# Kernel optimization log

Measured on AMD Instinct MI355X. Metric: run time of the kernel, lower is better.

## Reference

```python
import jax, jax.numpy as jnp
import numpy as np


def setup_inputs() -> dict:
    key = jax.random.key(0)
    ks = jax.random.split(key, 8)
    N, E, H, C, L, G = 100000, 1600000, 128, 10, 5, 64
    x = jax.random.normal(ks[0], (N, H), dtype=jnp.float32)
    edge_index = jax.random.randint(ks[1], (2, E), 0, N, dtype=jnp.int32)
    batch = jnp.sort(jax.random.randint(ks[2], (N,), 0, G, dtype=jnp.int32))
    # Glorot-ish init scale for stability
    Ws = jax.random.normal(ks[3], (L, H, H), dtype=jnp.float32) * (1.0 / np.sqrt(H))
    bs = jax.random.normal(ks[4], (L, H), dtype=jnp.float32) * 0.01
    W_out = jax.random.normal(ks[5], (H, C), dtype=jnp.float32) * (1.0 / np.sqrt(H))
    b_out = jax.random.normal(ks[6], (C,), dtype=jnp.float32) * 0.01
    return {"x": x, "edge_index": edge_index, "batch": batch, "num_graphs": G,
            "Ws": Ws, "bs": bs, "W_out": W_out, "b_out": b_out}


def reference(x, edge_index, batch, num_graphs, Ws, bs, W_out, b_out):
    N = x.shape[0]
    # --- GCN normalization (add self-loops, symmetric deg^-1/2 norm), computed once ---
    loop = jnp.arange(N, dtype=edge_index.dtype)
    src = jnp.concatenate([edge_index[0], loop])  # message sources (x_j)
    dst = jnp.concatenate([edge_index[1], loop])  # aggregation targets
    deg = jax.ops.segment_sum(jnp.ones_like(dst, dtype=x.dtype), dst, num_segments=N)
    dis = jnp.where(deg > 0, jax.lax.rsqrt(jnp.maximum(deg, 1.0)), 0.0)
    norm = dis[src] * dis[dst]  # [E+N]
    # --- stacked GCNConv + ReLU ---
    for l in range(Ws.shape[0]):
        xw = x @ Ws[l]                                   # [N, H] dense transform
        msg = norm[:, None] * xw[src]                    # gather + scale per edge
        x = jax.nn.relu(jax.ops.segment_sum(msg, dst, num_segments=N) + bs[l])
    # --- global mean pool over graphs ---
    sums = jax.ops.segment_sum(x, batch, num_segments=num_graphs)       # [G, H]
    cnts = jax.ops.segment_sum(jnp.ones((N,), x.dtype), batch, num_segments=num_graphs)
    pooled = sums / jnp.maximum(cnts, 1.0)[:, None]
    return pooled @ W_out + b_out
```

## Files before the change

kernel.cpp:

```cpp
#include <hip/hip_runtime.h>
#include <hip/hip_bf16.h>
#include <stdint.h>

#define HDIM 128
#define SBITS 10
#define SBMAX 128

typedef __attribute__((ext_vector_type(8))) short short8;
typedef __attribute__((ext_vector_type(4))) float f32x4;

__device__ __forceinline__ ushort f2bf(float f) {
  uint u = __float_as_uint(f);
  u = (u + 0x7fffu + ((u >> 16) & 1u)) >> 16;
  return (ushort)u;
}
__device__ __forceinline__ float bflo(uint v) { return __uint_as_float(v << 16); }
__device__ __forceinline__ float bfhi(uint v) { return __uint_as_float(v & 0xffff0000u); }

__device__ __forceinline__ int pdeg4(int c) { return (c + 4) & ~3; }

__device__ __forceinline__ uint pack_cw(int src, float w) {
  uint w15 = (__float_as_uint(w) + 0x8000u) >> 16;
  return (uint)src | (w15 << 17);
}
__device__ __forceinline__ uint cw_src(uint u) { return u & 0x1FFFFu; }
__device__ __forceinline__ float cw_w(uint u) { return __uint_as_float((u >> 17) << 16); }


__global__ __launch_bounds__(256) void bucket_edges(const int* __restrict__ ei,
                                                    int* __restrict__ bktcur,
                                                    uint* __restrict__ bkt, int E,
                                                    int cap) {
  __shared__ int hist[SBMAX], base[SBMAX];
  const int t = threadIdx.x;
  const int c0 = blockIdx.x * 2048;
  for (int i = t; i < SBMAX; i += 256) hist[i] = 0;
  __syncthreads();
  uint pk[8];
  int sb_[8], rk[8];
#pragma unroll
  for (int j = 0; j < 8; ++j) {
    int idx = c0 + j * 256 + t;
    sb_[j] = -1;
    if (idx < E) {
      int s = ei[idx];
      int d = ei[E + idx];
      int b = d >> SBITS;
      pk[j] = (uint)(d & 1023) | ((uint)s << SBITS);
      sb_[j] = b;
      rk[j] = atomicAdd(&hist[b], 1);
    }
  }
  __syncthreads();
  for (int i = t; i < SBMAX; i += 256)
    base[i] = hist[i] ? atomicAdd(&bktcur[i * 16], hist[i]) : 0;
  __syncthreads();
#pragma unroll
  for (int j = 0; j < 8; ++j)
    if (sb_[j] >= 0)
      bkt[(size_t)sb_[j] * cap + base[sb_[j]] + rk[j]] = pk[j];
}

__global__ __launch_bounds__(256) void csr_count(const uint* __restrict__ bkt,
                                                 const int* __restrict__ bktcur,
                                                 float* __restrict__ dis,
                                                 int* __restrict__ sbtot, int cap,
                                                 int N) {
  __shared__ int cnt[1024];
  __shared__ int red[256];
  const int sb = blockIdx.x, t = threadIdx.x;
  const int n0 = sb << SBITS;
  const int ecnt = bktcur[sb * 16];
  const uint* eb = bkt + (size_t)sb * cap;
  for (int i = t; i < 1024; i += 256) cnt[i] = 0;
  __syncthreads();
  for (int i = t; i < ecnt; i += 256)
    atomicAdd(&cnt[__builtin_nontemporal_load(eb + i) & 1023], 1);
  __syncthreads();
  int s = 0;
#pragma unroll
  for (int j = 0; j < 4; ++j) {
    int idx = t * 4 + j, n = n0 + idx;
    if (n < N) {
      dis[n] = rsqrtf((float)(cnt[idx] + 1));
      s += pdeg4(cnt[idx]);
    }
  }
  red[t] = s;
  __syncthreads();
  for (int off = 128; off; off >>= 1) {
    if (t < off) red[t] += red[t + off];
    __syncthreads();
  }
  if (t == 0) sbtot[sb] = red[0];
}

__global__ __launch_bounds__(128) void scan_sb(const int* __restrict__ sbtot,
                                               int* __restrict__ sbbase,
                                               int* __restrict__ rowptr, int SB,
                                               int N) {
  __shared__ int sh[128];
  int t = threadIdx.x;
  int v = (t < SB) ? sbtot[t] : 0;
  sh[t] = v;
  __syncthreads();
  for (int off = 1; off < 128; off <<= 1) {
    int add = (t >= off) ? sh[t - off] : 0;
    __syncthreads();
    sh[t] += add;
    __syncthreads();
  }
  if (t < SB) sbbase[t] = sh[t] - v;
  if (t == 127) rowptr[N] = sh[127];
}

__global__ __launch_bounds__(256) void csr_place(const uint* __restrict__ bkt,
                                                 const int* __restrict__ bktcur,
                                                 const int* __restrict__ sbbase,
                                                 const float* __restrict__ dis,
                                                 int* __restrict__ rowptr,
                                                 uint* __restrict__ colw, int cap,
                                                 int N) {
  __shared__ int cnt[1024], cur[1024];
  __shared__ int sh[256];
  const int sb = blockIdx.x, t = threadIdx.x;
  const int n0 = sb << SBITS;
  const int ecnt = bktcur[sb * 16];
  const uint* eb = bkt + (size_t)sb * cap;
  const int base = sbbase[sb];
  for (int i = t; i < 1024; i += 256) cnt[i] = 0;
  __syncthreads();
  for (int i = t; i < ecnt; i += 256)
    atomicAdd(&cnt[__builtin_nontemporal_load(eb + i) & 1023], 1);
  __syncthreads();
  int v[4], tsum = 0;
#pragma unroll
  for (int j = 0; j < 4; ++j) {
    int idx = t * 4 + j, n = n0 + idx;
    v[j] = (n < N) ? pdeg4(cnt[idx]) : 0;
    tsum += v[j];
  }
  sh[t] = tsum;
  __syncthreads();
  for (int off = 1; off < 256; off <<= 1) {
    int add = (t >= off) ? sh[t - off] : 0;
    __syncthreads();
    sh[t] += add;
    __syncthreads();
  }
  int p = sh[t] - tsum;
#pragma unroll
  for (int j = 0; j < 4; ++j) {
    int idx = t * 4 + j, n = n0 + idx;
    if (n < N) {
      rowptr[n] = base + p;
      cur[idx] = p + 1;
      float dn = dis[n];
      colw[base + p] = pack_cw(n, dn * dn);
      int deg = cnt[idx];
      for (int q = deg + 1; q < v[j]; ++q) colw[base + p + q] = (uint)n;
    }
    p += v[j];
  }
  __syncthreads();
  for (int i = t; i < ecnt; i += 256) {
    uint u = __builtin_nontemporal_load(eb + i);
    int dloc = (int)(u & 1023);
    int s2 = (int)(u >> SBITS);
    int pos = atomicAdd(&cur[dloc], 1);
    int d = n0 + dloc;
    colw[base + pos] = pack_cw(s2, dis[s2] * dis[d]);
  }
}

__global__ __launch_bounds__(256) void swz_w(const float* __restrict__ Ws,
                                             ushort* __restrict__ Wsw, int total) {
  int idx = blockIdx.x * 256 + threadIdx.x;
  if (idx >= total) return;
  int l = idx >> 14, r = idx & 16383;
  int j = r & 7, lane = (r >> 3) & 63, kk = (r >> 9) & 3, c = r >> 11;
  int n = c * 16 + (lane & 15);
  int k = kk * 32 + (lane >> 4) * 8 + j;
  Wsw[idx] = f2bf(Ws[l * 16384 + k * HDIM + n]);
}


template <bool F32IN>
__global__ __launch_bounds__(256) void gemm_kernel(const void* __restrict__ Xin,
                                                   const ushort* __restrict__ Wsw,
                                                   ushort* __restrict__ XW, int N,
                                                   int ntiles) {
  __shared__ ushort wlds[16384];
  __shared__ ushort clds[64 * 136];
  const int t = threadIdx.x;
  {
    const int4* src = (const int4*)Wsw;
    int4* dst = (int4*)wlds;
#pragma unroll
    for (int i = 0; i < 8; ++i) dst[t + 256 * i] = src[t + 256 * i];
  }
  __syncthreads();

  const int wave = t >> 6, lane = t & 63;
  const int kq = lane >> 4;

  for (int tile = blockIdx.x; tile < ntiles; tile += gridDim.x) {
    const int row0 = tile * 64 + wave * 16 + (lane & 15);
    const bool inb = row0 < N;

    short8 afr[4];
#pragma unroll
    for (int kk = 0; kk < 4; ++kk) afr[kk] = short8{0, 0, 0, 0, 0, 0, 0, 0};
    if (inb) {
      if constexpr (F32IN) {
        const float* arow = (const float*)Xin + (size_t)row0 * HDIM;
#pragma unroll
        for (int kk = 0; kk < 4; ++kk) {
          float4 x0 = *(const float4*)(arow + kk * 32 + kq * 8);
          float4 x1 = *(const float4*)(arow + kk * 32 + kq * 8 + 4);
          short8 f;
          f[0] = (short)f2bf(x0.x); f[1] = (short)f2bf(x0.y);
          f[2] = (short)f2bf(x0.z); f[3] = (short)f2bf(x0.w);
          f[4] = (short)f2bf(x1.x); f[5] = (short)f2bf(x1.y);
          f[6] = (short)f2bf(x1.z); f[7] = (short)f2bf(x1.w);
          afr[kk] = f;
        }
      } else {
        const short8* arow = (const short8*)((const ushort*)Xin + (size_t)row0 * HDIM);
#pragma unroll
        for (int kk = 0; kk < 4; ++kk) afr[kk] = arow[kk * 4 + kq];
      }
    }

    f32x4 acc[8];
#pragma unroll
    for (int c = 0; c < 8; ++c) acc[c] = f32x4{0.f, 0.f, 0.f, 0.f};
#pragma unroll
    for (int kk = 0; kk < 4; ++kk) {
#pragma unroll
      for (int c = 0; c < 8; ++c) {
        short8 bfr = *(const short8*)(wlds + (((c * 4 + kk) * 64 + lane) << 3));
        acc[c] = __builtin_amdgcn_mfma_f32_16x16x32_bf16(afr[kk], bfr, acc[c], 0, 0, 0);
      }
    }

    __syncthreads();
    const int m0 = wave * 16 + kq * 4;
#pragma unroll
    for (int c = 0; c < 8; ++c) {
      int col = c * 16 + (lane & 15);
#pragma unroll
      for (int r = 0; r < 4; ++r) clds[(m0 + r) * 136 + col] = f2bf(acc[c][r]);
    }
    __syncthreads();
#pragma unroll
    for (int i = 0; i < 4; ++i) {
      int idx = t + 256 * i;
      int row = idx >> 4, piece = idx & 15;
      int grow = tile * 64 + row;
      if (grow < N)
        ((int4*)XW)[(size_t)tile * 1024 + idx] =
            *(const int4*)(clds + row * 136 + piece * 8);
    }
  }
}

__global__ __launch_bounds__(256, 6) void agg_kernel(const ushort* __restrict__ XW,
                                                     const uint* __restrict__ colw,
                                                     const int* __restrict__ rowptr,
                                                     const float* __restrict__ bias,
                                                     ushort* __restrict__ Y, int N) {
  const int lane = threadIdx.x & 63;
  const int node = blockIdx.x * 4 + (threadIdx.x >> 6);
  if (node >= N) return;
  const int e = lane >> 4, c = lane & 15;
  const int beg = rowptr[node];
  const int pdeg = rowptr[node + 1] - beg;
  const int last = pdeg - 1;

  uint cw[6];
#pragma unroll
  for (int k = 0; k < 6; ++k) {
    int off = 4 * k + e;
    cw[k] = __builtin_nontemporal_load(colw + beg + (off < pdeg ? off : last));
  }
  uint4 gv[6];
#pragma unroll
  for (int k = 0; k < 6; ++k)
    gv[k] = *(const uint4*)(XW + ((size_t)cw_src(cw[k]) << 7) + c * 8);

  float acc[8];
#pragma unroll
  for (int i = 0; i < 8; ++i) acc[i] = 0.f;

#pragma unroll
  for (int k = 0; k < 6; ++k) {
    int off = 4 * k + e;
    float w = (off < pdeg) ? cw_w(cw[k]) : 0.f;
    uint4 v = gv[k];
    acc[0] += w * bflo(v.x); acc[1] += w * bfhi(v.x);
    acc[2] += w * bflo(v.y); acc[3] += w * bfhi(v.y);
    acc[4] += w * bflo(v.z); acc[5] += w * bfhi(v.z);
    acc[6] += w * bflo(v.w); acc[7] += w * bfhi(v.w);
  }
  for (int off = 24 + e; off < pdeg; off += 4) {
    uint u = __builtin_nontemporal_load(colw + beg + off);
    uint4 v = *(const uint4*)(XW + ((size_t)cw_src(u) << 7) + c * 8);
    float w = cw_w(u);
    acc[0] += w * bflo(v.x); acc[1] += w * bfhi(v.x);
    acc[2] += w * bflo(v.y); acc[3] += w * bfhi(v.y);
    acc[4] += w * bflo(v.z); acc[5] += w * bfhi(v.z);
    acc[6] += w * bflo(v.w); acc[7] += w * bfhi(v.w);
  }

#pragma unroll
  for (int i = 0; i < 8; ++i) {
    acc[i] += __shfl_xor(acc[i], 16, 64);
    acc[i] += __shfl_xor(acc[i], 32, 64);
  }
  if (e == 0) {
    float4 b0 = *(const float4*)(bias + c * 8);
    float4 b1 = *(const float4*)(bias + c * 8 + 4);
    uint4 pk;
    pk.x = (uint)f2bf(fmaxf(acc[0] + b0.x, 0.f)) | ((uint)f2bf(fmaxf(acc[1] + b0.y, 0.f)) << 16);
    pk.y = (uint)f2bf(fmaxf(acc[2] + b0.z, 0.f)) | ((uint)f2bf(fmaxf(acc[3] + b0.w, 0.f)) << 16);
    pk.z = (uint)f2bf(fmaxf(acc[4] + b1.x, 0.f)) | ((uint)f2bf(fmaxf(acc[5] + b1.y, 0.f)) << 16);
    pk.w = (uint)f2bf(fmaxf(acc[6] + b1.z, 0.f)) | ((uint)f2bf(fmaxf(acc[7] + b1.w, 0.f)) << 16);
    *(uint4*)(Y + (size_t)node * HDIM + c * 8) = pk;
  }
}


__global__ __launch_bounds__(256) void pool_partial(const ushort* __restrict__ x,
                                                    const int* __restrict__ batch,
                                                    float* __restrict__ pooled,
                                                    int* __restrict__ gcnt, int N) {
  const int g = blockIdx.x, s = blockIdx.y;
  const int t = threadIdx.x;
  __shared__ int range[2];
  __shared__ float sums[256];
  if (t < 2) {
    int target = g + t;
    int lo = 0, hi = N;
    while (lo < hi) {
      int mid = (lo + hi) >> 1;
      if (batch[mid] < target) lo = mid + 1;
      else hi = mid;
    }
    range[t] = lo;
  }
  __syncthreads();
  int beg = range[0], end = range[1];
  if (s == 0 && t == 0) gcnt[g] = end - beg;
  int col = t & 127, half = t >> 7;
  float acc = 0.f;
  for (int n = beg + s * 2 + half; n < end; n += 16) {
    acc += __uint_as_float(((uint)x[(size_t)n * HDIM + col]) << 16);
  }
  sums[t] = acc;
  __syncthreads();
  if (t < 128) atomicAdd(&pooled[g * HDIM + t], sums[t] + sums[t + 128]);
}

__global__ __launch_bounds__(256) void out_final(const float* __restrict__ pooled,
                                                 const int* __restrict__ gcnt,
                                                 const float* __restrict__ W_out,
                                                 const float* __restrict__ b_out,
                                                 float* __restrict__ out, int G, int C) {
  int i = blockIdx.x * 256 + threadIdx.x;
  if (i >= G * C) return;
  int g = i / C, c = i - g * C;
  float inv = 1.f / (float)max(gcnt[g], 1);
  const float* pg = pooled + g * HDIM;
  float o = 0.f;
  for (int h = 0; h < HDIM; ++h) o += pg[h] * W_out[h * C + c];
  out[i] = b_out[c] + o * inv;
}


extern "C" void kernel_launch(void* const* d_in, const int* in_sizes, int n_in,
                              void* d_out, int out_size, void* d_ws, size_t ws_size,
                              hipStream_t stream) {
  (void)n_in;
  (void)ws_size;
  const float* x = (const float*)d_in[0];
  const int* ei = (const int*)d_in[1];
  const int* batch = (const int*)d_in[2];
  const float* Ws = (const float*)d_in[4];
  const float* bs = (const float*)d_in[5];
  const float* W_out = (const float*)d_in[6];
  const float* b_out = (const float*)d_in[7];
  float* out = (float*)d_out;

  const int N = in_sizes[0] / HDIM;
  const int E = in_sizes[1] / 2;
  const int L = in_sizes[5] / HDIM;
  const int C = in_sizes[7];
  const int G = out_size / C;
  const int SB = (N + 1023) >> SBITS;
  const int cap = E / SB + 8192;

  char* p = (char*)d_ws;
  auto carve = [&](size_t bytes) {
    char* r = p;
    p += (bytes + 255) & ~(size_t)255;
    return r;
  };
  int* bktcur = (int*)carve(SBMAX * 64);
  float* dis = (float*)carve((size_t)N * 4);
  int* rowptr = (int*)carve((size_t)(N + 1) * 4);
  int* sbtot = (int*)carve(SBMAX * 4);
  int* sbbase = (int*)carve(SBMAX * 4);
  uint* bkt = (uint*)carve((size_t)SB * cap * 4);
  uint* colw = (uint*)carve(((size_t)E + 4 * (size_t)N + 64) * 4);
  ushort* Wsw = (ushort*)carve((size_t)L * HDIM * HDIM * 2);
  ushort* xw = (ushort*)carve((size_t)N * HDIM * 2);
  ushort* y0 = (ushort*)carve((size_t)N * HDIM * 2);
  ushort* y1 = (ushort*)carve((size_t)N * HDIM * 2);
  float* pooled = (float*)carve((size_t)G * HDIM * 4 + (size_t)G * 4);
  int* gcnt = (int*)(pooled + (size_t)G * HDIM);

  hipMemsetAsync(bktcur, 0, SBMAX * 64, stream);
  hipMemsetAsync(pooled, 0, (size_t)G * HDIM * 4 + (size_t)G * 4, stream);

  bucket_edges<<<(E + 2047) / 2048, 256, 0, stream>>>(ei, bktcur, bkt, E, cap);
  csr_count<<<SB, 256, 0, stream>>>(bkt, bktcur, dis, sbtot, cap, N);
  scan_sb<<<1, 128, 0, stream>>>(sbtot, sbbase, rowptr, SB, N);
  csr_place<<<SB, 256, 0, stream>>>(bkt, bktcur, sbbase, dis, rowptr, colw, cap, N);
  swz_w<<<(L * HDIM * HDIM + 255) / 256, 256, 0, stream>>>(Ws, Wsw, L * HDIM * HDIM);

  const int ntiles = (N + 63) / 64;
  const int gb = 768;
  gemm_kernel<true><<<gb, 256, 0, stream>>>(x, Wsw, xw, N, ntiles);
  agg_kernel<<<(N + 3) / 4, 256, 0, stream>>>(xw, colw, rowptr, bs, y0, N);
  ushort* xc = y0;
  ushort* xn = y1;
  for (int l = 1; l < L; ++l) {
    gemm_kernel<false><<<gb, 256, 0, stream>>>(xc, Wsw + (size_t)l * HDIM * HDIM, xw, N, ntiles);
    agg_kernel<<<(N + 3) / 4, 256, 0, stream>>>(xw, colw, rowptr, bs + (size_t)l * HDIM, xn, N);
    ushort* tmp = xc;
    xc = xn;
    xn = tmp;
  }
  pool_partial<<<dim3(G, 8), 256, 0, stream>>>(xc, batch, pooled, gcnt, N);
  out_final<<<(G * C + 255) / 256, 256, 0, stream>>>(pooled, gcnt, W_out, b_out, out, G, C);
}
```

Baseline: 573.5 us.

## Fuse aggregation and GEMM per layer by reassociating A(XW) as (AX)W

Uses linearity to aggregate the input features first and then apply the weight matrix in the same kernel. Each block gathers 64 nodes into LDS, with a two-node software pipeline that overlaps gathers, then runs the MFMA GEMM and applies bias plus ReLU before writing out. This removes the intermediate XW round trip through global memory and one launch per layer, and the input is converted to bf16 once up front. In exchange, occupancy drops (launch bounds 3, large LDS footprint), each block must reload the weights, and the GEMM now runs on a bf16-rounded aggregate, which changes rounding.

```diff
diff --git a/kernel.cpp b/kernel.cpp
--- a/kernel.cpp
+++ b/kernel.cpp
@@ -184,149 +184,155 @@
   Wsw[idx] = f2bf(Ws[l * 16384 + k * HDIM + n]);
 }
 
-
-template <bool F32IN>
-__global__ __launch_bounds__(256) void gemm_kernel(const void* __restrict__ Xin,
-                                                   const ushort* __restrict__ Wsw,
-                                                   ushort* __restrict__ XW, int N,
-                                                   int ntiles) {
-  __shared__ ushort wlds[16384];
-  __shared__ ushort clds[64 * 136];
-  const int t = threadIdx.x;
-  {
-    const int4* src = (const int4*)Wsw;
-    int4* dst = (int4*)wlds;
-#pragma unroll
-    for (int i = 0; i < 8; ++i) dst[t + 256 * i] = src[t + 256 * i];
-  }
-  __syncthreads();
-
-  const int wave = t >> 6, lane = t & 63;
-  const int kq = lane >> 4;
-
-  for (int tile = blockIdx.x; tile < ntiles; tile += gridDim.x) {
-    const int row0 = tile * 64 + wave * 16 + (lane & 15);
-    const bool inb = row0 < N;
-
-    short8 afr[4];
-#pragma unroll
-    for (int kk = 0; kk < 4; ++kk) afr[kk] = short8{0, 0, 0, 0, 0, 0, 0, 0};
-    if (inb) {
-      if constexpr (F32IN) {
-        const float* arow = (const float*)Xin + (size_t)row0 * HDIM;
-#pragma unroll
-        for (int kk = 0; kk < 4; ++kk) {
-          float4 x0 = *(const float4*)(arow + kk * 32 + kq * 8);
-          float4 x1 = *(const float4*)(arow + kk * 32 + kq * 8 + 4);
-          short8 f;
-          f[0] = (short)f2bf(x0.x); f[1] = (short)f2bf(x0.y);
-          f[2] = (short)f2bf(x0.z); f[3] = (short)f2bf(x0.w);
-          f[4] = (short)f2bf(x1.x); f[5] = (short)f2bf(x1.y);
-          f[6] = (short)f2bf(x1.z); f[7] = (short)f2bf(x1.w);
-          afr[kk] = f;
-        }
-      } else {
-        const short8* arow = (const short8*)((const ushort*)Xin + (size_t)row0 * HDIM);
-#pragma unroll
-        for (int kk = 0; kk < 4; ++kk) afr[kk] = arow[kk * 4 + kq];
-      }
-    }
-
-    f32x4 acc[8];
-#pragma unroll
-    for (int c = 0; c < 8; ++c) acc[c] = f32x4{0.f, 0.f, 0.f, 0.f};
-#pragma unroll
-    for (int kk = 0; kk < 4; ++kk) {
-#pragma unroll
-      for (int c = 0; c < 8; ++c) {
-        short8 bfr = *(const short8*)(wlds + (((c * 4 + kk) * 64 + lane) << 3));
-        acc[c] = __builtin_amdgcn_mfma_f32_16x16x32_bf16(afr[kk], bfr, acc[c], 0, 0, 0);
-      }
-    }
-
-    __syncthreads();
-    const int m0 = wave * 16 + kq * 4;
-#pragma unroll
-    for (int c = 0; c < 8; ++c) {
-      int col = c * 16 + (lane & 15);
-#pragma unroll
-      for (int r = 0; r < 4; ++r) clds[(m0 + r) * 136 + col] = f2bf(acc[c][r]);
-    }
-    __syncthreads();
-#pragma unroll
-    for (int i = 0; i < 4; ++i) {
-      int idx = t + 256 * i;
-      int row = idx >> 4, piece = idx & 15;
-      int grow = tile * 64 + row;
-      if (grow < N)
-        ((int4*)XW)[(size_t)tile * 1024 + idx] =
-            *(const int4*)(clds + row * 136 + piece * 8);
-    }
-  }
-}
-
-__global__ __launch_bounds__(256, 6) void agg_kernel(const ushort* __restrict__ XW,
-                                                     const uint* __restrict__ colw,
-                                                     const int* __restrict__ rowptr,
-                                                     const float* __restrict__ bias,
-                                                     ushort* __restrict__ Y, int N) {
-  const int lane = threadIdx.x & 63;
-  const int node = blockIdx.x * 4 + (threadIdx.x >> 6);
-  if (node >= N) return;
-  const int e = lane >> 4, c = lane & 15;
-  const int beg = rowptr[node];
-  const int pdeg = rowptr[node + 1] - beg;
-  const int last = pdeg - 1;
-
-  uint cw[6];
+__global__ __launch_bounds__(256) void cvt_x(const float* __restrict__ x,
+                                             ushort* __restrict__ xb, int total) {
+  int i = (blockIdx.x * 256 + threadIdx.x) * 4;
+  if (i < total) {
+    float4 v = *(const float4*)(x + i);
+    uint2 o;
+    o.x = (uint)f2bf(v.x) | ((uint)f2bf(v.y) << 16);
+    o.y = (uint)f2bf(v.z) | ((uint)f2bf(v.w) << 16);
+    *(uint2*)(xb + i) = o;
+  }
+}
+
+
+__device__ __forceinline__ void issue_node(const ushort* __restrict__ Xin,
+                                           const uint* __restrict__ colw,
+                                           const int* __restrict__ rowptr,
+                                           int node, int N, int e, int c,
+                                           uint (&cw)[6], uint4 (&gv)[6],
+                                           int& beg, int& pd) {
+  if (node < N) {
+    beg = rowptr[node];
+    pd = rowptr[node + 1] - beg;
+  } else {
+    beg = 0;
+    pd = 0;
+  }
+  const int last = pd > 0 ? pd - 1 : 0;
 #pragma unroll
   for (int k = 0; k < 6; ++k) {
     int off = 4 * k + e;
-    cw[k] = __builtin_nontemporal_load(colw + beg + (off < pdeg ? off : last));
-  }
-  uint4 gv[6];
+    cw[k] = pd ? __builtin_nontemporal_load(colw + beg + (off < pd ? off : last))
+               : 0u;
+  }
 #pragma unroll
   for (int k = 0; k < 6; ++k)
-    gv[k] = *(const uint4*)(XW + ((size_t)cw_src(cw[k]) << 7) + c * 8);
-
+    gv[k] = *(const uint4*)(Xin + ((size_t)cw_src(cw[k]) << 7) + c * 8);
+}
+
+__device__ __forceinline__ void consume_node(const ushort* __restrict__ Xin,
+                                             const uint* __restrict__ colw,
+                                             ushort* __restrict__ zlds, int row,
+                                             int beg, int pd, int e, int c,
+                                             const uint (&cw)[6],
+                                             const uint4 (&gv)[6]) {
   float acc[8];
 #pragma unroll
   for (int i = 0; i < 8; ++i) acc[i] = 0.f;
-
 #pragma unroll
   for (int k = 0; k < 6; ++k) {
     int off = 4 * k + e;
-    float w = (off < pdeg) ? cw_w(cw[k]) : 0.f;
+    float w = (off < pd) ? cw_w(cw[k]) : 0.f;
     uint4 v = gv[k];
     acc[0] += w * bflo(v.x); acc[1] += w * bfhi(v.x);
     acc[2] += w * bflo(v.y); acc[3] += w * bfhi(v.y);
     acc[4] += w * bflo(v.z); acc[5] += w * bfhi(v.z);
     acc[6] += w * bflo(v.w); acc[7] += w * bfhi(v.w);
   }
-  for (int off = 24 + e; off < pdeg; off += 4) {
+  for (int off = 24 + e; off < pd; off += 4) {
     uint u = __builtin_nontemporal_load(colw + beg + off);
-    uint4 v = *(const uint4*)(XW + ((size_t)cw_src(u) << 7) + c * 8);
+    uint4 v = *(const uint4*)(Xin + ((size_t)cw_src(u) << 7) + c * 8);
     float w = cw_w(u);
     acc[0] += w * bflo(v.x); acc[1] += w * bfhi(v.x);
     acc[2] += w * bflo(v.y); acc[3] += w * bfhi(v.y);
     acc[4] += w * bflo(v.z); acc[5] += w * bfhi(v.z);
     acc[6] += w * bflo(v.w); acc[7] += w * bfhi(v.w);
   }
-
 #pragma unroll
   for (int i = 0; i < 8; ++i) {
     acc[i] += __shfl_xor(acc[i], 16, 64);
     acc[i] += __shfl_xor(acc[i], 32, 64);
   }
   if (e == 0) {
-    float4 b0 = *(const float4*)(bias + c * 8);
-    float4 b1 = *(const float4*)(bias + c * 8 + 4);
     uint4 pk;
-    pk.x = (uint)f2bf(fmaxf(acc[0] + b0.x, 0.f)) | ((uint)f2bf(fmaxf(acc[1] + b0.y, 0.f)) << 16);
-    pk.y = (uint)f2bf(fmaxf(acc[2] + b0.z, 0.f)) | ((uint)f2bf(fmaxf(acc[3] + b0.w, 0.f)) << 16);
-    pk.z = (uint)f2bf(fmaxf(acc[4] + b1.x, 0.f)) | ((uint)f2bf(fmaxf(acc[5] + b1.y, 0.f)) << 16);
-    pk.w = (uint)f2bf(fmaxf(acc[6] + b1.z, 0.f)) | ((uint)f2bf(fmaxf(acc[7] + b1.w, 0.f)) << 16);
-    *(uint4*)(Y + (size_t)node * HDIM + c * 8) = pk;
+    pk.x = (uint)f2bf(acc[0]) | ((uint)f2bf(acc[1]) << 16);
+    pk.y = (uint)f2bf(acc[2]) | ((uint)f2bf(acc[3]) << 16);
+    pk.z = (uint)f2bf(acc[4]) | ((uint)f2bf(acc[5]) << 16);
+    pk.w = (uint)f2bf(acc[6]) | ((uint)f2bf(acc[7]) << 16);
+    *(uint4*)(zlds + row * 136 + c * 8) = pk;
+  }
+}
+
+__global__ __launch_bounds__(256, 3) void agg_gemm(
+    const ushort* __restrict__ Xin, const uint* __restrict__ colw,
+    const int* __restrict__ rowptr, const ushort* __restrict__ Wsw,
+    const float* __restrict__ bias, ushort* __restrict__ Xout, int N) {
+  __shared__ ushort wlds[16384];
+  __shared__ ushort zlds[64 * 136];
+  const int t = threadIdx.x;
+  {
+    const int4* src = (const int4*)Wsw;
+    int4* dst = (int4*)wlds;
+#pragma unroll
+    for (int i = 0; i < 8; ++i) dst[t + 256 * i] = src[t + 256 * i];
+  }
+  const int wave = t >> 6, lane = t & 63;
+  const int e = lane >> 4, c = lane & 15;
+  const int nbase = blockIdx.x * 64 + wave * 16;
+
+  uint cwA[6], cwB[6];
+  uint4 gvA[6], gvB[6];
+  int begA, pdA, begB, pdB;
+  issue_node(Xin, colw, rowptr, nbase + 0, N, e, c, cwA, gvA, begA, pdA);
+  for (int i = 0; i < 16; i += 2) {
+    issue_node(Xin, colw, rowptr, nbase + i + 1, N, e, c, cwB, gvB, begB, pdB);
+    consume_node(Xin, colw, zlds, wave * 16 + i, begA, pdA, e, c, cwA, gvA);
+    if (i + 2 < 16)
+      issue_node(Xin, colw, rowptr, nbase + i + 2, N, e, c, cwA, gvA, begA, pdA);
+    consume_node(Xin, colw, zlds, wave * 16 + i + 1, begB, pdB, e, c, cwB, gvB);
+  }
+  __syncthreads();
+
+  const int kq = lane >> 4;
+  const int arow = wave * 16 + (lane & 15);
+  short8 afr[4];
+#pragma unroll
+  for (int kk = 0; kk < 4; ++kk)
+    afr[kk] = *(const short8*)(zlds + arow * 136 + kk * 32 + kq * 8);
+  __syncthreads();
+
+  f32x4 acc[8];
+#pragma unroll
+  for (int cc = 0; cc < 8; ++cc) acc[cc] = f32x4{0.f, 0.f, 0.f, 0.f};
+#pragma unroll
+  for (int kk = 0; kk < 4; ++kk) {
+#pragma unroll
+    for (int cc = 0; cc < 8; ++cc) {
+      short8 bfr = *(const short8*)(wlds + (((cc * 4 + kk) * 64 + lane) << 3));
+      acc[cc] = __builtin_amdgcn_mfma_f32_16x16x32_bf16(afr[kk], bfr, acc[cc], 0, 0, 0);
+    }
+  }
+
+  const int m0 = wave * 16 + kq * 4;
+#pragma unroll
+  for (int cc = 0; cc < 8; ++cc) {
+    int col = cc * 16 + (lane & 15);
+    float bv = bias[col];
+#pragma unroll
+    for (int r = 0; r < 4; ++r)
+      zlds[(m0 + r) * 136 + col] = f2bf(fmaxf(acc[cc][r] + bv, 0.f));
+  }
+  __syncthreads();
+#pragma unroll
+  for (int i = 0; i < 4; ++i) {
+    int idx = t + 256 * i;
+    int row = idx >> 4, piece = idx & 15;
+    int grow = blockIdx.x * 64 + row;
+    if (grow < N)
+      ((int4*)Xout)[(size_t)blockIdx.x * 1024 + idx] =
+          *(const int4*)(zlds + row * 136 + piece * 8);
   }
 }
 
@@ -414,7 +420,7 @@
   uint* bkt = (uint*)carve((size_t)SB * cap * 4);
   uint* colw = (uint*)carve(((size_t)E + 4 * (size_t)N + 64) * 4);
   ushort* Wsw = (ushort*)carve((size_t)L * HDIM * HDIM * 2);
-  ushort* xw = (ushort*)carve((size_t)N * HDIM * 2);
+  ushort* xa = (ushort*)carve((size_t)N * HDIM * 2);
   ushort* y0 = (ushort*)carve((size_t)N * HDIM * 2);
   ushort* y1 = (ushort*)carve((size_t)N * HDIM * 2);
   float* pooled = (float*)carve((size_t)G * HDIM * 4 + (size_t)G * 4);
@@ -428,19 +434,17 @@
   scan_sb<<<1, 128, 0, stream>>>(sbtot, sbbase, rowptr, SB, N);
   csr_place<<<SB, 256, 0, stream>>>(bkt, bktcur, sbbase, dis, rowptr, colw, cap, N);
   swz_w<<<(L * HDIM * HDIM + 255) / 256, 256, 0, stream>>>(Ws, Wsw, L * HDIM * HDIM);
-
-  const int ntiles = (N + 63) / 64;
-  const int gb = 768;
-  gemm_kernel<true><<<gb, 256, 0, stream>>>(x, Wsw, xw, N, ntiles);
-  agg_kernel<<<(N + 3) / 4, 256, 0, stream>>>(xw, colw, rowptr, bs, y0, N);
-  ushort* xc = y0;
-  ushort* xn = y1;
-  for (int l = 1; l < L; ++l) {
-    gemm_kernel<false><<<gb, 256, 0, stream>>>(xc, Wsw + (size_t)l * HDIM * HDIM, xw, N, ntiles);
-    agg_kernel<<<(N + 3) / 4, 256, 0, stream>>>(xw, colw, rowptr, bs + (size_t)l * HDIM, xn, N);
-    ushort* tmp = xc;
+  cvt_x<<<((N * HDIM / 4) + 255) / 256, 256, 0, stream>>>(x, xa, N * HDIM);
+
+  const int gb = (N + 63) / 64;
+  ushort* xc = xa;
+  ushort* ybuf[2] = {y0, y1};
+  for (int l = 0; l < L; ++l) {
+    ushort* xn = ybuf[l & 1];
+    agg_gemm<<<gb, 256, 0, stream>>>(xc, colw, rowptr,
+                                     Wsw + (size_t)l * HDIM * HDIM,
+                                     bs + (size_t)l * HDIM, xn, N);
     xc = xn;
-    xn = tmp;
   }
   pool_partial<<<dim3(G, 8), 256, 0, stream>>>(xc, batch, pooled, gcnt, N);
   out_final<<<(G * C + 255) / 256, 256, 0, stream>>>(pooled, gcnt, W_out, b_out, out, G, C);
```

Measured after the change: 694.5 us. +21.1%, slower.
